# Optimization experiments

Hardware: AMD Instinct MI355X
Metric: run time of the kernel (lower is better)

## Reference

```python
import jax, jax.numpy as jnp
import numpy as np

INPUT_SIZE = 1
HIDDEN = 50
OUTPUT = 1
BATCH = 2048
SEQ = 512


def _lstm_layer(x, W_ih, W_hh, b_ih, b_hh):
    # x: [B, T, I]; W_ih: [4H, I]; W_hh: [4H, H]; biases: [4H]
    B = x.shape[0]
    H = W_hh.shape[1]
    # Precompute input contributions for all timesteps: [B, T, 4H]
    xg = jnp.einsum('bti,gi->btg', x, W_ih) + b_ih + b_hh

    def step(carry, xg_t):
        h, c = carry                      # [B, H] each
        g = xg_t + h @ W_hh.T             # [B, 4H]
        i, f, gg, o = jnp.split(g, 4, axis=-1)  # PyTorch gate order i,f,g,o
        i = jax.nn.sigmoid(i)
        f = jax.nn.sigmoid(f)
        gg = jnp.tanh(gg)
        o = jax.nn.sigmoid(o)
        c = f * c + i * gg
        h = o * jnp.tanh(c)
        return (h, c), h

    h0 = jnp.zeros((B, H), x.dtype)
    c0 = jnp.zeros((B, H), x.dtype)
    _, hs = jax.lax.scan(step, (h0, c0), jnp.swapaxes(xg, 0, 1))  # hs: [T, B, H]
    return jnp.swapaxes(hs, 0, 1)  # [B, T, H]


def setup_inputs() -> dict:
    key = jax.random.key(0)
    ks = jax.random.split(key, 11)
    s = 1.0 / np.sqrt(HIDDEN)  # PyTorch LSTM init scale
    x = jax.random.normal(ks[0], (BATCH, SEQ, INPUT_SIZE), dtype=jnp.float32)
    W_ih0 = jax.random.uniform(ks[1], (4 * HIDDEN, INPUT_SIZE), minval=-s, maxval=s)
    W_hh0 = jax.random.uniform(ks[2], (4 * HIDDEN, HIDDEN), minval=-s, maxval=s)
    b_ih0 = jax.random.uniform(ks[3], (4 * HIDDEN,), minval=-s, maxval=s)
    b_hh0 = jax.random.uniform(ks[4], (4 * HIDDEN,), minval=-s, maxval=s)
    W_ih1 = jax.random.uniform(ks[5], (4 * HIDDEN, HIDDEN), minval=-s, maxval=s)
    W_hh1 = jax.random.uniform(ks[6], (4 * HIDDEN, HIDDEN), minval=-s, maxval=s)
    b_ih1 = jax.random.uniform(ks[7], (4 * HIDDEN,), minval=-s, maxval=s)
    b_hh1 = jax.random.uniform(ks[8], (4 * HIDDEN,), minval=-s, maxval=s)
    fc_W = jax.random.uniform(ks[9], (OUTPUT, HIDDEN), minval=-s, maxval=s)
    fc_b = jax.random.uniform(ks[10], (OUTPUT,), minval=-s, maxval=s)
    return {
        'x': x,
        'W_ih0': W_ih0, 'W_hh0': W_hh0, 'b_ih0': b_ih0, 'b_hh0': b_hh0,
        'W_ih1': W_ih1, 'W_hh1': W_hh1, 'b_ih1': b_ih1, 'b_hh1': b_hh1,
        'fc_W': fc_W, 'fc_b': fc_b,
    }


def reference(x, W_ih0, W_hh0, b_ih0, b_hh0, W_ih1, W_hh1, b_ih1, b_hh1, fc_W, fc_b):
    h1 = _lstm_layer(x, W_ih0, W_hh0, b_ih0, b_hh0)   # [B, T, H]
    h2 = _lstm_layer(h1, W_ih1, W_hh1, b_ih1, b_hh1)  # [B, T, H]
    last = h2[:, -1, :]                               # [B, H]
    return last @ fc_W.T + fc_b                       # [B, OUTPUT]
```

## Files before the change

### kernel.cpp

```cpp
#include <hip/hip_runtime.h>

typedef _Float16 f16x8 __attribute__((ext_vector_type(8)));
typedef float    f32x4 __attribute__((ext_vector_type(4)));

constexpr int BATCH = 2048;
constexpr int SEQ   = 512;
constexpr int H     = 50;
constexpr int NB    = 8;
constexpr int NT    = 1024;
constexpr int KQ    = 4;
constexpr int PSZ   = KQ * 64 * 8;

__device__ __forceinline__ float fexp2(float x) { return __builtin_amdgcn_exp2f(x); }
__device__ __forceinline__ float frcp(float x)  { return __builtin_amdgcn_rcpf(x); }
__device__ __forceinline__ _Float16 f16hi(float w) { return (_Float16)w; }
__device__ __forceinline__ _Float16 f16lo(float w) {
    _Float16 h = (_Float16)w; return (_Float16)(w - (float)h);
}
__device__ __forceinline__ int baddr(int k, int n) {
    return (((k >> 5) * 64) + (((k >> 3) & 3) * 16) + n) * 8 + (k & 7);
}
union H2U { unsigned u; _Float16 h[2]; };

constexpr float K1 = 1.4426950408889634f;
constexpr float K2 = 2.8853900817779268f;


__global__ __launch_bounds__(NT, 4) void lstm2_hi(
    const float* __restrict__ x,
    const float* __restrict__ Wih0, const float* __restrict__ Whh0,
    const float* __restrict__ bih0, const float* __restrict__ bhh0,
    const float* __restrict__ Wih1, const float* __restrict__ Whh1,
    const float* __restrict__ bih1, const float* __restrict__ bhh1,
    const float* __restrict__ fcW,  const float* __restrict__ fcb,
    float* __restrict__ out)
{
    __shared__ _Float16 sB[2][PSZ];
    __shared__ unsigned sXu[SEQ * NB];
    __shared__ float    sH2f[H * NB];

    const int t    = threadIdx.x;
    const int wave = t >> 6, lane = t & 63;
    const int quad = lane >> 4, nn = lane & 15;
    const int bbase = blockIdx.x * NB;

    for (int i = t; i < 2 * PSZ; i += NT) ((_Float16*)sB)[i] = (_Float16)0.f;

    for (int i = t; i < NB * SEQ; i += NT) {
        const int b = i >> 9, s = i & (SEQ - 1);
        float xv = x[(bbase + b) * SEQ + s];
        H2U p; p.h[0] = f16hi(xv); p.h[1] = f16lo(xv);
        sXu[s * NB + b] = p.u;
    }

    const bool mmv = (wave < 13);
    f16x8 a0[2];
    f16x8 a1[KQ];
    f32x4 b0v = {0,0,0,0}, b1v = {0,0,0,0};
    if (mmv) {
        const int  m    = wave;
        const int  jr   = m * 4 + (nn >> 2);
        const int  gate = nn & 3;
        const bool rv   = (jr < H);
        const int  lrow = gate * H + jr;
        #pragma unroll
        for (int q = 0; q < 2; ++q) {
            #pragma unroll
            for (int j = 0; j < 8; ++j) {
                const int k = q * 32 + quad * 8 + j;
                _Float16 v = (_Float16)0.f;
                if (rv) {
                    if      (k < 50)   v = (_Float16)Whh0[lrow * H + k];
                    else if (k == 50)  v = f16hi(Wih0[lrow]);
                    else if (k == 51)  v = f16lo(Wih0[lrow]);
                }
                a0[q][j] = v;
            }
        }
        #pragma unroll
        for (int q = 0; q < KQ; ++q) {
            #pragma unroll
            for (int j = 0; j < 8; ++j) {
                const int k = q * 32 + quad * 8 + j;
                _Float16 v = (_Float16)0.f;
                if (rv) {
                    if      (k < 50)              v = (_Float16)Wih1[lrow * H + k];
                    else if (k >= 64 && k < 114)  v = (_Float16)Whh1[lrow * H + (k - 64)];
                }
                a1[q][j] = v;
            }
        }
        const int jq = m * 4 + quad;
        #pragma unroll
        for (int r = 0; r < 4; ++r) {
            const bool bv = (jq < H);
            b0v[r] = bv ? (bih0[r * H + jq] + bhh0[r * H + jq]) : 0.f;
            b1v[r] = bv ? (bih1[r * H + jq] + bhh1[r * H + jq]) : 0.f;
        }
    }

    const int  jj   = wave * 4 + quad;
    const bool hiH  = (nn >= 8);
    const int  col  = nn & 7;
    const int  kb   = hiH ? (64 + jj) : jj;
    const int  wH0  = baddr(kb, col);
    const int  wH1  = baddr(kb, col + 8);
    const bool wrOK = mmv && (jj < H);
    float c = 0.f;

    const int xcol = lane & 7;
    const int xad  = baddr(50, (lane & 7) + 8 * ((lane >> 3) & 1)) >> 1;

    __syncthreads();
    if (t < 16)
        ((unsigned*)sB[0])[baddr(50, (t & 7) + 8 * (t >> 3)) >> 1] = sXu[t & 7];
    __syncthreads();

    auto body = [&](int s, const _Float16* __restrict__ br,
                    _Float16* __restrict__ bw,
                    bool doL0, bool doL1, bool doX, bool last) {
        if (mmv) {
            f16x8 bq[KQ];
            #pragma unroll
            for (int q = 0; q < KQ; ++q)
                bq[q] = *(const f16x8*)&br[(q * 64 + lane) * 8];

            f32x4 g0 = b0v;
            #pragma unroll
            for (int q = 0; q < 2; ++q)
                g0 = __builtin_amdgcn_mfma_f32_16x16x32_f16(a0[q], bq[q], g0, 0, 0, 0);
            f32x4 g1 = b1v;
            #pragma unroll
            for (int q = 0; q < KQ; ++q)
                g1 = __builtin_amdgcn_mfma_f32_16x16x32_f16(a1[q], bq[q], g1, 0, 0, 0);

            f32x4 g;
            #pragma unroll
            for (int r = 0; r < 4; ++r) g[r] = hiH ? g1[r] : g0[r];

            const bool act = hiH ? doL1 : doL0;
            if (act) {
                float Ei = fexp2(-K1 * g[0]);
                float Ef = fexp2(-K1 * g[1]);
                float Eg = fexp2(-K2 * fabsf(g[2]));
                float Eo = fexp2(-K1 * g[3]);
                float it = copysignf((1.f - Eg) * frcp((1.f + Ei) * (1.f + Eg)), g[2]);
                c = frcp(1.f + Ef) * c + it;
                float Ec = fexp2(-K2 * fabsf(c));
                float h  = copysignf((1.f - Ec) * frcp((1.f + Eo) * (1.f + Ec)), c);
                if (wrOK) {
                    if (last && hiH) {
                        sH2f[jj * NB + col] = h;
                    } else {
                        _Float16 hh = (_Float16)h;
                        bw[wH0] = hh;
                        bw[wH1] = hh;
                    }
                }
            }
        } else if (doX && wave == 15 && lane < 16) {
            ((unsigned*)bw)[xad] = sXu[(s + 1) * NB + xcol];
        }
        __syncthreads();
    };

    body(0, sB[0], sB[1], true, false, true, false);
    #pragma unroll 1
    for (int i = 0; i < 255; ++i) {
        body(2 * i + 1, sB[1], sB[0], true, true, true, false);
        body(2 * i + 2, sB[0], sB[1], true, true, true, false);
    }
    body(511, sB[1], sB[0], true, true, false, false);
    body(512, sB[0], sB[1], false, true, false, true);

    if (t < NB) {
        float sum = fcb[0];
        #pragma unroll
        for (int jx = 0; jx < H; ++jx) sum += fcW[jx] * sH2f[jx * NB + t];
        out[bbase + t] = sum;
    }
}

extern "C" void kernel_launch(void* const* d_in, const int* in_sizes, int n_in,
                              void* d_out, int out_size, void* d_ws, size_t ws_size,
                              hipStream_t stream)
{
    const float* x    = (const float*)d_in[0];
    const float* Wih0 = (const float*)d_in[1];
    const float* Whh0 = (const float*)d_in[2];
    const float* bih0 = (const float*)d_in[3];
    const float* bhh0 = (const float*)d_in[4];
    const float* Wih1 = (const float*)d_in[5];
    const float* Whh1 = (const float*)d_in[6];
    const float* bih1 = (const float*)d_in[7];
    const float* bhh1 = (const float*)d_in[8];
    const float* fcW  = (const float*)d_in[9];
    const float* fcb  = (const float*)d_in[10];

    lstm2_hi<<<BATCH / NB, NT, 0, stream>>>(
        x, Wih0, Whh0, bih0, bhh0, Wih1, Whh1, bih1, bhh1, fcW, fcb,
        (float*)d_out);
}
```

Baseline: 321.9 us.

## Split LSTM layers across dedicated waves and add input term in fp32

Waves are split so waves 0-6 compute only layer 0 and waves 7-13 only layer 1. Each wave handles two 4-unit tiles, so no MFMA work is spent on the unused layer. The input projection for layer 0 moves out of the MFMA K dimension into an fp32 FMA that reads x from shared memory. This removes the per-step x-injection wave and the hi/lo fp16 split. Block size drops from 1024 to 896 threads, but each wave now issues more MFMAs per step on the layer-1 path, which may lengthen the critical per-step latency.

```diff
diff --git a/kernel.cpp b/kernel.cpp
--- a/kernel.cpp
+++ b/kernel.cpp
@@ -7,26 +7,21 @@
 constexpr int SEQ   = 512;
 constexpr int H     = 50;
 constexpr int NB    = 8;
-constexpr int NT    = 1024;
+constexpr int NT    = 896;
 constexpr int KQ    = 4;
 constexpr int PSZ   = KQ * 64 * 8;
 
 __device__ __forceinline__ float fexp2(float x) { return __builtin_amdgcn_exp2f(x); }
 __device__ __forceinline__ float frcp(float x)  { return __builtin_amdgcn_rcpf(x); }
-__device__ __forceinline__ _Float16 f16hi(float w) { return (_Float16)w; }
-__device__ __forceinline__ _Float16 f16lo(float w) {
-    _Float16 h = (_Float16)w; return (_Float16)(w - (float)h);
-}
 __device__ __forceinline__ int baddr(int k, int n) {
     return (((k >> 5) * 64) + (((k >> 3) & 3) * 16) + n) * 8 + (k & 7);
 }
-union H2U { unsigned u; _Float16 h[2]; };
 
 constexpr float K1 = 1.4426950408889634f;
 constexpr float K2 = 2.8853900817779268f;
 
 
-__global__ __launch_bounds__(NT, 4) void lstm2_hi(
+__global__ __launch_bounds__(NT, 4) void lstm2_split(
     const float* __restrict__ x,
     const float* __restrict__ Wih0, const float* __restrict__ Whh0,
     const float* __restrict__ bih0, const float* __restrict__ bhh0,
@@ -36,7 +31,7 @@
     float* __restrict__ out)
 {
     __shared__ _Float16 sB[2][PSZ];
-    __shared__ unsigned sXu[SEQ * NB];
+    __shared__ float    sX32[SEQ * NB];
     __shared__ float    sH2f[H * NB];
 
     const int t    = threadIdx.x;
@@ -45,111 +40,135 @@
     const int bbase = blockIdx.x * NB;
 
     for (int i = t; i < 2 * PSZ; i += NT) ((_Float16*)sB)[i] = (_Float16)0.f;
-
     for (int i = t; i < NB * SEQ; i += NT) {
         const int b = i >> 9, s = i & (SEQ - 1);
-        float xv = x[(bbase + b) * SEQ + s];
-        H2U p; p.h[0] = f16hi(xv); p.h[1] = f16lo(xv);
-        sXu[s * NB + b] = p.u;
-    }
-
-    const bool mmv = (wave < 13);
-    f16x8 a0[2];
-    f16x8 a1[KQ];
-    f32x4 b0v = {0,0,0,0}, b1v = {0,0,0,0};
-    if (mmv) {
-        const int  m    = wave;
-        const int  jr   = m * 4 + (nn >> 2);
+        sX32[s * NB + b] = x[(bbase + b) * SEQ + s];
+    }
+
+    const bool isL0 = (wave < 7);
+    const int  g    = isL0 ? wave : wave - 7;
+    const bool t2v  = (8 * g + 4 < H);
+
+    f16x8 a0[2][2];
+    f16x8 a1[2][4];
+    f32x4 bv[2];
+    #pragma unroll
+    for (int i = 0; i < 2; ++i) {
+        const int  ti   = 2 * g + i;
+        const int  jr   = ti * 4 + (nn >> 2);
         const int  gate = nn & 3;
         const bool rv   = (jr < H);
         const int  lrow = gate * H + jr;
-        #pragma unroll
-        for (int q = 0; q < 2; ++q) {
-            #pragma unroll
-            for (int j = 0; j < 8; ++j) {
-                const int k = q * 32 + quad * 8 + j;
-                _Float16 v = (_Float16)0.f;
-                if (rv) {
-                    if      (k < 50)   v = (_Float16)Whh0[lrow * H + k];
-                    else if (k == 50)  v = f16hi(Wih0[lrow]);
-                    else if (k == 51)  v = f16lo(Wih0[lrow]);
-                }
-                a0[q][j] = v;
-            }
+        if (isL0) {
+            #pragma unroll
+            for (int q = 0; q < 2; ++q)
+                #pragma unroll
+                for (int j = 0; j < 8; ++j) {
+                    const int k = q * 32 + quad * 8 + j;
+                    a0[i][q][j] = (rv && k < 50) ? (_Float16)Whh0[lrow * H + k]
+                                                 : (_Float16)0.f;
+                }
+        } else {
+            #pragma unroll
+            for (int q = 0; q < 4; ++q)
+                #pragma unroll
+                for (int j = 0; j < 8; ++j) {
+                    const int k = q * 32 + quad * 8 + j;
+                    _Float16 v = (_Float16)0.f;
+                    if (rv) {
+                        if      (k < 50)              v = (_Float16)Wih1[lrow * H + k];
+                        else if (k >= 64 && k < 114)  v = (_Float16)Whh1[lrow * H + (k - 64)];
+                    }
+                    a1[i][q][j] = v;
+                }
         }
-        #pragma unroll
-        for (int q = 0; q < KQ; ++q) {
-            #pragma unroll
-            for (int j = 0; j < 8; ++j) {
-                const int k = q * 32 + quad * 8 + j;
-                _Float16 v = (_Float16)0.f;
-                if (rv) {
-                    if      (k < 50)              v = (_Float16)Wih1[lrow * H + k];
-                    else if (k >= 64 && k < 114)  v = (_Float16)Whh1[lrow * H + (k - 64)];
-                }
-                a1[q][j] = v;
-            }
-        }
-        const int jq = m * 4 + quad;
+        const int jq = ti * 4 + quad;
         #pragma unroll
         for (int r = 0; r < 4; ++r) {
-            const bool bv = (jq < H);
-            b0v[r] = bv ? (bih0[r * H + jq] + bhh0[r * H + jq]) : 0.f;
-            b1v[r] = bv ? (bih1[r * H + jq] + bhh1[r * H + jq]) : 0.f;
+            const bool bvv = (jq < H);
+            bv[i][r] = !bvv ? 0.f
+                     : (isL0 ? (bih0[r * H + jq] + bhh0[r * H + jq])
+                             : (bih1[r * H + jq] + bhh1[r * H + jq]));
         }
     }
 
-    const int  jj   = wave * 4 + quad;
-    const bool hiH  = (nn >= 8);
+    const bool hiT  = (nn >= 8);
+    const int  jj   = 8 * g + (hiT ? 4 : 0) + quad;
     const int  col  = nn & 7;
-    const int  kb   = hiH ? (64 + jj) : jj;
+    const bool wrOK = (jj < H);
+    const int  kb   = isL0 ? jj : (64 + jj);
     const int  wH0  = baddr(kb, col);
     const int  wH1  = baddr(kb, col + 8);
-    const bool wrOK = mmv && (jj < H);
+    float wx[4];
+    #pragma unroll
+    for (int r = 0; r < 4; ++r)
+        wx[r] = (isL0 && wrOK) ? Wih0[r * H + jj] : 0.f;
     float c = 0.f;
 
-    const int xcol = lane & 7;
-    const int xad  = baddr(50, (lane & 7) + 8 * ((lane >> 3) & 1)) >> 1;
-
-    __syncthreads();
-    if (t < 16)
-        ((unsigned*)sB[0])[baddr(50, (t & 7) + 8 * (t >> 3)) >> 1] = sXu[t & 7];
     __syncthreads();
 
     auto body = [&](int s, const _Float16* __restrict__ br,
                     _Float16* __restrict__ bw,
-                    bool doL0, bool doL1, bool doX, bool last) {
-        if (mmv) {
-            f16x8 bq[KQ];
-            #pragma unroll
-            for (int q = 0; q < KQ; ++q)
-                bq[q] = *(const f16x8*)&br[(q * 64 + lane) * 8];
-
-            f32x4 g0 = b0v;
-            #pragma unroll
-            for (int q = 0; q < 2; ++q)
-                g0 = __builtin_amdgcn_mfma_f32_16x16x32_f16(a0[q], bq[q], g0, 0, 0, 0);
-            f32x4 g1 = b1v;
-            #pragma unroll
-            for (int q = 0; q < KQ; ++q)
-                g1 = __builtin_amdgcn_mfma_f32_16x16x32_f16(a1[q], bq[q], g1, 0, 0, 0);
-
-            f32x4 g;
-            #pragma unroll
-            for (int r = 0; r < 4; ++r) g[r] = hiH ? g1[r] : g0[r];
-
-            const bool act = hiH ? doL1 : doL0;
-            if (act) {
-                float Ei = fexp2(-K1 * g[0]);
-                float Ef = fexp2(-K1 * g[1]);
-                float Eg = fexp2(-K2 * fabsf(g[2]));
-                float Eo = fexp2(-K1 * g[3]);
-                float it = copysignf((1.f - Eg) * frcp((1.f + Ei) * (1.f + Eg)), g[2]);
+                    bool doL0, bool doL1, bool last) {
+        if (isL0) {
+            f16x8 b0 = *(const f16x8*)&br[(0 * 64 + lane) * 8];
+            f16x8 b1 = *(const f16x8*)&br[(1 * 64 + lane) * 8];
+            f32x4 A = bv[0], B = bv[1];
+            A = __builtin_amdgcn_mfma_f32_16x16x32_f16(a0[0][0], b0, A, 0, 0, 0);
+            A = __builtin_amdgcn_mfma_f32_16x16x32_f16(a0[0][1], b1, A, 0, 0, 0);
+            if (t2v) {
+                B = __builtin_amdgcn_mfma_f32_16x16x32_f16(a0[1][0], b0, B, 0, 0, 0);
+                B = __builtin_amdgcn_mfma_f32_16x16x32_f16(a0[1][1], b1, B, 0, 0, 0);
+            }
+            if (doL0) {
+                f32x4 gg;
+                #pragma unroll
+                for (int r = 0; r < 4; ++r) gg[r] = hiT ? B[r] : A[r];
+                const float xv = sX32[s * NB + col];
+                #pragma unroll
+                for (int r = 0; r < 4; ++r) gg[r] = fmaf(wx[r], xv, gg[r]);
+                float Ei = fexp2(-K1 * gg[0]);
+                float Ef = fexp2(-K1 * gg[1]);
+                float Eg = fexp2(-K2 * fabsf(gg[2]));
+                float Eo = fexp2(-K1 * gg[3]);
+                float it = copysignf((1.f - Eg) * frcp((1.f + Ei) * (1.f + Eg)), gg[2]);
                 c = frcp(1.f + Ef) * c + it;
                 float Ec = fexp2(-K2 * fabsf(c));
                 float h  = copysignf((1.f - Ec) * frcp((1.f + Eo) * (1.f + Ec)), c);
                 if (wrOK) {
-                    if (last && hiH) {
+                    _Float16 hh = (_Float16)h;
+                    bw[wH0] = hh;
+                    bw[wH1] = hh;
+                }
+            }
+        } else {
+            f16x8 bq[4];
+            #pragma unroll
+            for (int q = 0; q < 4; ++q)
+                bq[q] = *(const f16x8*)&br[(q * 64 + lane) * 8];
+            f32x4 A = bv[0], B = bv[1];
+            #pragma unroll
+            for (int q = 0; q < 4; ++q)
+                A = __builtin_amdgcn_mfma_f32_16x16x32_f16(a1[0][q], bq[q], A, 0, 0, 0);
+            if (t2v) {
+                #pragma unroll
+                for (int q = 0; q < 4; ++q)
+                    B = __builtin_amdgcn_mfma_f32_16x16x32_f16(a1[1][q], bq[q], B, 0, 0, 0);
+            }
+            if (doL1) {
+                f32x4 gg;
+                #pragma unroll
+                for (int r = 0; r < 4; ++r) gg[r] = hiT ? B[r] : A[r];
+                float Ei = fexp2(-K1 * gg[0]);
+                float Ef = fexp2(-K1 * gg[1]);
+                float Eg = fexp2(-K2 * fabsf(gg[2]));
+                float Eo = fexp2(-K1 * gg[3]);
+                float it = copysignf((1.f - Eg) * frcp((1.f + Ei) * (1.f + Eg)), gg[2]);
+                c = frcp(1.f + Ef) * c + it;
+                float Ec = fexp2(-K2 * fabsf(c));
+                float h  = copysignf((1.f - Ec) * frcp((1.f + Eo) * (1.f + Ec)), c);
+                if (wrOK) {
+                    if (last) {
                         sH2f[jj * NB + col] = h;
                     } else {
                         _Float16 hh = (_Float16)h;
@@ -158,20 +177,18 @@
                     }
                 }
             }
-        } else if (doX && wave == 15 && lane < 16) {
-            ((unsigned*)bw)[xad] = sXu[(s + 1) * NB + xcol];
         }
         __syncthreads();
     };
 
-    body(0, sB[0], sB[1], true, false, true, false);
+    body(0, sB[0], sB[1], true, false, false);
     #pragma unroll 1
     for (int i = 0; i < 255; ++i) {
-        body(2 * i + 1, sB[1], sB[0], true, true, true, false);
-        body(2 * i + 2, sB[0], sB[1], true, true, true, false);
-    }
-    body(511, sB[1], sB[0], true, true, false, false);
-    body(512, sB[0], sB[1], false, true, false, true);
+        body(2 * i + 1, sB[1], sB[0], true, true, false);
+        body(2 * i + 2, sB[0], sB[1], true, true, false);
+    }
+    body(511, sB[1], sB[0], true, true, false);
+    body(512, sB[0], sB[1], false, true, true);
 
     if (t < NB) {
         float sum = fcb[0];
@@ -197,7 +214,7 @@
     const float* fcW  = (const float*)d_in[9];
     const float* fcb  = (const float*)d_in[10];
 
-    lstm2_hi<<<BATCH / NB, NT, 0, stream>>>(
+    lstm2_split<<<BATCH / NB, NT, 0, stream>>>(
         x, Wih0, Whh0, bih0, bhh0, Wih1, Whh1, bih1, bhh1, fcW, fcb,
         (float*)d_out);
 }
```

Result: slower. 351.7 us (+9.3%).

## Share one K=64 state buffer across both layers using DPP cross-lane gate combine

Applied to the files above, without the earlier changes.

Both layers' hidden states now live in a single K=64 operand buffer: h1 occupies columns 0-7 and h2 columns 8-15. Layer 1's input term is computed in separate MFMAs and moved across lanes with a DPP row rotate. The input x is added in fp32 via fma instead of being packed as f16 hi/lo into the MFMA operand, which removes the x-injection wave and the duplicate h writes. This halves shared-memory reads per step and shortens the MFMA dependency chain, at the cost of a DPP move per gate.

```diff
diff --git a/kernel.cpp b/kernel.cpp
--- a/kernel.cpp
+++ b/kernel.cpp
@@ -8,25 +8,26 @@
 constexpr int H     = 50;
 constexpr int NB    = 8;
 constexpr int NT    = 1024;
-constexpr int KQ    = 4;
+constexpr int KQ    = 2;
 constexpr int PSZ   = KQ * 64 * 8;
 
 __device__ __forceinline__ float fexp2(float x) { return __builtin_amdgcn_exp2f(x); }
 __device__ __forceinline__ float frcp(float x)  { return __builtin_amdgcn_rcpf(x); }
-__device__ __forceinline__ _Float16 f16hi(float w) { return (_Float16)w; }
-__device__ __forceinline__ _Float16 f16lo(float w) {
-    _Float16 h = (_Float16)w; return (_Float16)(w - (float)h);
-}
 __device__ __forceinline__ int baddr(int k, int n) {
     return (((k >> 5) * 64) + (((k >> 3) & 3) * 16) + n) * 8 + (k & 7);
 }
-union H2U { unsigned u; _Float16 h[2]; };
+union FI { float f; int i; };
+__device__ __forceinline__ float dpp_xor8(float v) {
+    FI u; u.f = v;
+    FI r; r.i = __builtin_amdgcn_mov_dpp(u.i, 0x128, 0xf, 0xf, true);
+    return r.f;
+}
 
 constexpr float K1 = 1.4426950408889634f;
 constexpr float K2 = 2.8853900817779268f;
 
 
-__global__ __launch_bounds__(NT, 4) void lstm2_hi(
+__global__ __launch_bounds__(NT, 4) void lstm2_cs(
     const float* __restrict__ x,
     const float* __restrict__ Wih0, const float* __restrict__ Whh0,
     const float* __restrict__ bih0, const float* __restrict__ bhh0,
@@ -36,7 +37,7 @@
     float* __restrict__ out)
 {
     __shared__ _Float16 sB[2][PSZ];
-    __shared__ unsigned sXu[SEQ * NB];
+    __shared__ float    sX32[SEQ * NB];
     __shared__ float    sH2f[H * NB];
 
     const int t    = threadIdx.x;
@@ -45,17 +46,15 @@
     const int bbase = blockIdx.x * NB;
 
     for (int i = t; i < 2 * PSZ; i += NT) ((_Float16*)sB)[i] = (_Float16)0.f;
-
     for (int i = t; i < NB * SEQ; i += NT) {
         const int b = i >> 9, s = i & (SEQ - 1);
-        float xv = x[(bbase + b) * SEQ + s];
-        H2U p; p.h[0] = f16hi(xv); p.h[1] = f16lo(xv);
-        sXu[s * NB + b] = p.u;
+        sX32[s * NB + b] = x[(bbase + b) * SEQ + s];
     }
 
     const bool mmv = (wave < 13);
-    f16x8 a0[2];
-    f16x8 a1[KQ];
+    f16x8 a0[KQ];
+    f16x8 aP[KQ];
+    f16x8 aQ[KQ];
     f32x4 b0v = {0,0,0,0}, b1v = {0,0,0,0};
     if (mmv) {
         const int  m    = wave;
@@ -64,30 +63,14 @@
         const bool rv   = (jr < H);
         const int  lrow = gate * H + jr;
         #pragma unroll
-        for (int q = 0; q < 2; ++q) {
-            #pragma unroll
-            for (int j = 0; j < 8; ++j) {
-                const int k = q * 32 + quad * 8 + j;
-                _Float16 v = (_Float16)0.f;
-                if (rv) {
-                    if      (k < 50)   v = (_Float16)Whh0[lrow * H + k];
-                    else if (k == 50)  v = f16hi(Wih0[lrow]);
-                    else if (k == 51)  v = f16lo(Wih0[lrow]);
-                }
-                a0[q][j] = v;
-            }
-        }
-        #pragma unroll
         for (int q = 0; q < KQ; ++q) {
             #pragma unroll
             for (int j = 0; j < 8; ++j) {
                 const int k = q * 32 + quad * 8 + j;
-                _Float16 v = (_Float16)0.f;
-                if (rv) {
-                    if      (k < 50)              v = (_Float16)Wih1[lrow * H + k];
-                    else if (k >= 64 && k < 114)  v = (_Float16)Whh1[lrow * H + (k - 64)];
-                }
-                a1[q][j] = v;
+                const bool kv = rv && (k < 50);
+                a0[q][j] = kv ? (_Float16)Whh0[lrow * H + k] : (_Float16)0.f;
+                aP[q][j] = kv ? (_Float16)Wih1[lrow * H + k] : (_Float16)0.f;
+                aQ[q][j] = kv ? (_Float16)Whh1[lrow * H + k] : (_Float16)0.f;
             }
         }
         const int jq = m * 4 + quad;
@@ -102,41 +85,41 @@
     const int  jj   = wave * 4 + quad;
     const bool hiH  = (nn >= 8);
     const int  col  = nn & 7;
-    const int  kb   = hiH ? (64 + jj) : jj;
-    const int  wH0  = baddr(kb, col);
-    const int  wH1  = baddr(kb, col + 8);
     const bool wrOK = mmv && (jj < H);
+    const int  wH   = baddr(jj, nn);
+    float wx[4];
+    #pragma unroll
+    for (int r = 0; r < 4; ++r)
+        wx[r] = wrOK ? Wih0[r * H + jj] : 0.f;
     float c = 0.f;
 
-    const int xcol = lane & 7;
-    const int xad  = baddr(50, (lane & 7) + 8 * ((lane >> 3) & 1)) >> 1;
-
-    __syncthreads();
-    if (t < 16)
-        ((unsigned*)sB[0])[baddr(50, (t & 7) + 8 * (t >> 3)) >> 1] = sXu[t & 7];
     __syncthreads();
 
     auto body = [&](int s, const _Float16* __restrict__ br,
                     _Float16* __restrict__ bw,
-                    bool doL0, bool doL1, bool doX, bool last) {
+                    bool doL0, bool doL1, bool last) {
         if (mmv) {
-            f16x8 bq[KQ];
-            #pragma unroll
-            for (int q = 0; q < KQ; ++q)
-                bq[q] = *(const f16x8*)&br[(q * 64 + lane) * 8];
+            f16x8 b0 = *(const f16x8*)&br[(0 * 64 + lane) * 8];
+            f16x8 b1 = *(const f16x8*)&br[(1 * 64 + lane) * 8];
 
             f32x4 g0 = b0v;
-            #pragma unroll
-            for (int q = 0; q < 2; ++q)
-                g0 = __builtin_amdgcn_mfma_f32_16x16x32_f16(a0[q], bq[q], g0, 0, 0, 0);
-            f32x4 g1 = b1v;
-            #pragma unroll
-            for (int q = 0; q < KQ; ++q)
-                g1 = __builtin_amdgcn_mfma_f32_16x16x32_f16(a1[q], bq[q], g1, 0, 0, 0);
+            g0 = __builtin_amdgcn_mfma_f32_16x16x32_f16(a0[0], b0, g0, 0, 0, 0);
+            g0 = __builtin_amdgcn_mfma_f32_16x16x32_f16(a0[1], b1, g0, 0, 0, 0);
+            f32x4 P = {0.f, 0.f, 0.f, 0.f};
+            P = __builtin_amdgcn_mfma_f32_16x16x32_f16(aP[0], b0, P, 0, 0, 0);
+            P = __builtin_amdgcn_mfma_f32_16x16x32_f16(aP[1], b1, P, 0, 0, 0);
+            f32x4 Q = b1v;
+            Q = __builtin_amdgcn_mfma_f32_16x16x32_f16(aQ[0], b0, Q, 0, 0, 0);
+            Q = __builtin_amdgcn_mfma_f32_16x16x32_f16(aQ[1], b1, Q, 0, 0, 0);
 
+            const float xv = sX32[s * NB + col];
             f32x4 g;
             #pragma unroll
-            for (int r = 0; r < 4; ++r) g[r] = hiH ? g1[r] : g0[r];
+            for (int r = 0; r < 4; ++r) {
+                float gHi = Q[r] + dpp_xor8(P[r]);
+                float gLo = fmaf(wx[r], xv, g0[r]);
+                g[r] = hiH ? gHi : gLo;
+            }
 
             const bool act = hiH ? doL1 : doL0;
             if (act) {
@@ -149,29 +132,22 @@
                 float Ec = fexp2(-K2 * fabsf(c));
                 float h  = copysignf((1.f - Ec) * frcp((1.f + Eo) * (1.f + Ec)), c);
                 if (wrOK) {
-                    if (last && hiH) {
-                        sH2f[jj * NB + col] = h;
-                    } else {
-                        _Float16 hh = (_Float16)h;
-                        bw[wH0] = hh;
-                        bw[wH1] = hh;
-                    }
+                    if (last && hiH) sH2f[jj * NB + col] = h;
+                    else             bw[wH] = (_Float16)h;
                 }
             }
-        } else if (doX && wave == 15 && lane < 16) {
-            ((unsigned*)bw)[xad] = sXu[(s + 1) * NB + xcol];
         }
         __syncthreads();
     };
 
-    body(0, sB[0], sB[1], true, false, true, false);
+    body(0, sB[0], sB[1], true, false, false);
     #pragma unroll 1
     for (int i = 0; i < 255; ++i) {
-        body(2 * i + 1, sB[1], sB[0], true, true, true, false);
-        body(2 * i + 2, sB[0], sB[1], true, true, true, false);
+        body(2 * i + 1, sB[1], sB[0], true, true, false);
+        body(2 * i + 2, sB[0], sB[1], true, true, false);
     }
-    body(511, sB[1], sB[0], true, true, false, false);
-    body(512, sB[0], sB[1], false, true, false, true);
+    body(511, sB[1], sB[0], true, true, false);
+    body(512, sB[0], sB[1], false, true, true);
 
     if (t < NB) {
         float sum = fcb[0];
@@ -197,7 +173,7 @@
     const float* fcW  = (const float*)d_in[9];
     const float* fcb  = (const float*)d_in[10];
 
-    lstm2_hi<<<BATCH / NB, NT, 0, stream>>>(
+    lstm2_cs<<<BATCH / NB, NT, 0, stream>>>(
         x, Wih0, Whh0, bih0, bhh0, Wih1, Whh1, bih1, bhh1, fcW, fcb,
         (float*)d_out);
 }
```

New measurement: 344.2 us. 6.9% more time.
